# Kernel tuning notes

Hardware: AMD Instinct MI355X
Metric: run time of the kernel (lower is better)

## Reference

```python
import jax, jax.numpy as jnp
import numpy as np

N_NODES = 100000
N_EDGES = 600000
IN_FEAT = 128
OUT_FEAT = 128
NUM_RELS = 8
NUM_BASES = 4


def setup_inputs() -> dict:
    key = jax.random.key(0)
    ks = jax.random.split(key, 8)
    h = jax.random.normal(ks[0], (N_NODES, IN_FEAT), dtype=jnp.float32)
    # xavier-ish scale for params
    weight = jax.random.normal(ks[1], (NUM_BASES, IN_FEAT, OUT_FEAT), dtype=jnp.float32) * (1.0 / np.sqrt(IN_FEAT))
    w_comp = jax.random.normal(ks[2], (NUM_RELS, NUM_BASES), dtype=jnp.float32) * (1.0 / np.sqrt(NUM_BASES))
    root_weight = jax.random.normal(ks[3], (IN_FEAT, OUT_FEAT), dtype=jnp.float32) * (1.0 / np.sqrt(IN_FEAT))
    bias = jnp.zeros((OUT_FEAT,), dtype=jnp.float32)
    src = jax.random.randint(ks[4], (N_EDGES,), 0, N_NODES, dtype=jnp.int32)
    dst = jax.random.randint(ks[5], (N_EDGES,), 0, N_NODES, dtype=jnp.int32)
    rel_type = jax.random.randint(ks[6], (N_EDGES,), 0, NUM_RELS, dtype=jnp.int32)
    return {"h": h, "weight": weight, "w_comp": w_comp, "root_weight": root_weight,
            "bias": bias, "src": src, "dst": dst, "rel_type": rel_type}


def reference(h, weight, w_comp, root_weight, bias, src, dst, rel_type):
    # Basis decomposition: W[r] = sum_b w_comp[r,b] * weight[b]
    B, I, O = weight.shape
    R = w_comp.shape[0]
    W = (w_comp @ weight.reshape(B, I * O)).reshape(R, I, O)  # [R, in, out]
    # msg_e = h[src_e] @ W[rel_e]; computed as all-relation projection + gather
    # (avoids materializing [E, in, out] per-edge weights)
    proj = jnp.einsum('ni,rio->nro', h, W)          # [N, R, out]
    msg = proj[src, rel_type]                        # [E, out]
    agg = jax.ops.segment_sum(msg, dst, num_segments=h.shape[0])  # scatter-sum
    out = h @ root_weight + agg + bias
    return jax.nn.relu(out)
```

## Files before the change

### kernel.cpp

```cpp
#include <hip/hip_runtime.h>
#include <hip/hip_bf16.h>

#define N_NODES 100000
#define N_EDGES 600000
#define FEAT 128
#define NUM_RELS 8
#define NUM_BASES 4
#define NBE 2344

#define PREP_CAST 6250
#define PREP_BLDB 320
#define PREP_ZERO 392
#define PREP_GRID (PREP_CAST + PREP_BLDB + PREP_ZERO)

#define SCAN_TILES 98

typedef short bf16x8 __attribute__((ext_vector_type(8)));
typedef float f32x4  __attribute__((ext_vector_type(4)));
typedef float f32x2  __attribute__((ext_vector_type(2)));

__device__ inline short f2bf(float x) {
    __hip_bfloat16 b = __float2bfloat16(x);
    return *reinterpret_cast<short*>(&b);
}


__global__ __launch_bounds__(256) void k_prep(const float* __restrict__ h,
                                              const float* __restrict__ weight,
                                              const float* __restrict__ rw,
                                              short* __restrict__ hb,
                                              short* __restrict__ Btf,
                                              int* __restrict__ cnt,
                                              int* __restrict__ status) {
    int b = blockIdx.x;
    if (b < PREP_CAST) {
        int i = b * 256 + threadIdx.x;
        const float4* h4 = (const float4*)h;
        float4 v0 = h4[2 * i], v1 = h4[2 * i + 1];
        union { short s[8]; bf16x8 v; } u;
        u.s[0] = f2bf(v0.x); u.s[1] = f2bf(v0.y); u.s[2] = f2bf(v0.z); u.s[3] = f2bf(v0.w);
        u.s[4] = f2bf(v1.x); u.s[5] = f2bf(v1.y); u.s[6] = f2bf(v1.z); u.s[7] = f2bf(v1.w);
        ((bf16x8*)hb)[i] = u.v;
    } else if (b < PREP_CAST + PREP_BLDB) {
        int idx = (b - PREP_CAST) * 256 + threadIdx.x;
        int kc = idx >> 14;
        int e  = idx & 16383;
        int o  = e >> 7, ip = e & 127;
        float v = (kc == 0) ? rw[ip * FEAT + o]
                            : weight[(kc - 1) * FEAT * FEAT + ip * FEAT + o];
        int nt = o & 7, n16 = o >> 3;
        int ks = ip >> 5, quad = (ip >> 3) & 3, j = ip & 7;
        int lane = quad * 16 + n16;
        Btf[((kc * 4 + ks) * 8 + nt) * 512 + lane * 8 + j] = f2bf(v);
    } else {
        int i = (b - PREP_CAST - PREP_BLDB) * 256 + threadIdx.x;
        if (i < N_NODES) cnt[i] = 0;
        else if (i - N_NODES < 128) status[i - N_NODES] = 0;
    }
}

__global__ __launch_bounds__(256) void k_hist_dst(const int* __restrict__ dst,
                                                  int* __restrict__ cnt) {
    int i = blockIdx.x * 256 + threadIdx.x;
    if (i < N_EDGES) atomicAdd(&cnt[dst[i]], 1);
}

__global__ __launch_bounds__(256) void k_scan_lb(const int* __restrict__ cnt,
                                                 int* __restrict__ offs,
                                                 int* __restrict__ cursor,
                                                 int* __restrict__ status) {
    __shared__ int wsum[4];
    __shared__ int bcast;
    int bid = blockIdx.x;
    int lane = threadIdx.x & 63, wid = threadIdx.x >> 6;
    const int N4 = N_NODES / 4;
    int i4 = bid * 256 + threadIdx.x;

    const int4* cnt4 = (const int4*)cnt;
    int4 v = (i4 < N4) ? cnt4[i4] : make_int4(0, 0, 0, 0);
    int s = v.x + v.y + v.z + v.w;
    int incl = s;
#pragma unroll
    for (int d = 1; d < 64; d <<= 1) {
        int t = __shfl_up(incl, d);
        if (lane >= d) incl += t;
    }
    if (lane == 63) wsum[wid] = incl;
    __syncthreads();
    if (threadIdx.x == 0) {
        int a = 0;
#pragma unroll
        for (int w = 0; w < 4; ++w) { int x = wsum[w]; wsum[w] = a; a += x; }
        int total = a;
        __hip_atomic_store(&status[bid], (total << 2) | 1,
                           __ATOMIC_RELEASE, __HIP_MEMORY_SCOPE_AGENT);
        int excl = 0;
        for (int t = bid - 1; t >= 0; ) {
            int st = __hip_atomic_load(&status[t],
                                       __ATOMIC_ACQUIRE, __HIP_MEMORY_SCOPE_AGENT);
            if ((st & 3) == 0) { __builtin_amdgcn_s_sleep(1); continue; }
            excl += st >> 2;
            if ((st & 3) == 2) break;
            --t;
        }
        __hip_atomic_store(&status[bid], ((excl + total) << 2) | 2,
                           __ATOMIC_RELEASE, __HIP_MEMORY_SCOPE_AGENT);
        bcast = excl;
        if (bid == SCAN_TILES - 1) offs[N_NODES] = excl + total;
    }
    __syncthreads();
    int base = bcast + wsum[wid] + incl - s;
    if (i4 < N4) {
        int4 ex;
        ex.x = base;
        ex.y = base + v.x;
        ex.z = base + v.x + v.y;
        ex.w = base + v.x + v.y + v.z;
        ((int4*)offs)[i4]   = ex;
        ((int4*)cursor)[i4] = ex;
    }
}

__global__ __launch_bounds__(256) void k_scatter_sorted(const int* __restrict__ src,
                                                        const int* __restrict__ dst,
                                                        const int* __restrict__ rel,
                                                        int* __restrict__ cursor,
                                                        int* __restrict__ packed) {
    int e = blockIdx.x * 256 + threadIdx.x;
    if (e < N_EDGES) {
        int p = atomicAdd(&cursor[dst[e]], 1);
        packed[p] = (src[e] << 3) | rel[e];
    }
}

__global__ __launch_bounds__(256) void k_edge_z(const int* __restrict__ offs,
                                                const int* __restrict__ packed,
                                                const float* __restrict__ wc,
                                                const short* __restrict__ hb,
                                                unsigned int* __restrict__ z_u32) {
    int wid = threadIdx.x >> 6, lane = threadIdx.x & 63;
    int d = blockIdx.x * 4 + wid;
    if (d >= N_NODES) return;
    int s = offs[d], e = offs[d + 1];

    const float4* wc4 = (const float4*)wc;
    const unsigned int* hbu = (const unsigned int*)hb;

    f32x2 z2[4] = {(f32x2)0.f, (f32x2)0.f, (f32x2)0.f, (f32x2)0.f};

    for (int base = s; base < e; base += 64) {
        int rem = e - base;
        int m = rem < 64 ? rem : 64;
        int pk = (lane < m) ? packed[base + lane] : 0;
        int j = 0;
        for (; j + 3 < m; j += 4) {
            int p0 = __builtin_amdgcn_readlane(pk, j);
            int p1 = __builtin_amdgcn_readlane(pk, j + 1);
            int p2 = __builtin_amdgcn_readlane(pk, j + 2);
            int p3 = __builtin_amdgcn_readlane(pk, j + 3);
            unsigned int v0 = hbu[(size_t)(p0 >> 3) * 64 + lane];
            unsigned int v1 = hbu[(size_t)(p1 >> 3) * 64 + lane];
            unsigned int v2 = hbu[(size_t)(p2 >> 3) * 64 + lane];
            unsigned int v3 = hbu[(size_t)(p3 >> 3) * 64 + lane];
            float4 c0 = wc4[p0 & 7];
            float4 c1 = wc4[p1 & 7];
            float4 c2 = wc4[p2 & 7];
            float4 c3 = wc4[p3 & 7];
            f32x2 h0; h0.x = __int_as_float(v0 << 16); h0.y = __int_as_float(v0 & 0xffff0000u);
            f32x2 h1; h1.x = __int_as_float(v1 << 16); h1.y = __int_as_float(v1 & 0xffff0000u);
            f32x2 h2; h2.x = __int_as_float(v2 << 16); h2.y = __int_as_float(v2 & 0xffff0000u);
            f32x2 h3; h3.x = __int_as_float(v3 << 16); h3.y = __int_as_float(v3 & 0xffff0000u);
            f32x2 cc;
            cc = c0.x; z2[0] += cc * h0;
            cc = c0.y; z2[1] += cc * h0;
            cc = c0.z; z2[2] += cc * h0;
            cc = c0.w; z2[3] += cc * h0;
            cc = c1.x; z2[0] += cc * h1;
            cc = c1.y; z2[1] += cc * h1;
            cc = c1.z; z2[2] += cc * h1;
            cc = c1.w; z2[3] += cc * h1;
            cc = c2.x; z2[0] += cc * h2;
            cc = c2.y; z2[1] += cc * h2;
            cc = c2.z; z2[2] += cc * h2;
            cc = c2.w; z2[3] += cc * h2;
            cc = c3.x; z2[0] += cc * h3;
            cc = c3.y; z2[1] += cc * h3;
            cc = c3.z; z2[2] += cc * h3;
            cc = c3.w; z2[3] += cc * h3;
        }
        for (; j < m; ++j) {
            int p0 = __builtin_amdgcn_readlane(pk, j);
            unsigned int v0 = hbu[(size_t)(p0 >> 3) * 64 + lane];
            float4 c0 = wc4[p0 & 7];
            f32x2 h0; h0.x = __int_as_float(v0 << 16); h0.y = __int_as_float(v0 & 0xffff0000u);
            f32x2 cc;
            cc = c0.x; z2[0] += cc * h0;
            cc = c0.y; z2[1] += cc * h0;
            cc = c0.z; z2[2] += cc * h0;
            cc = c0.w; z2[3] += cc * h0;
        }
    }

    unsigned int* row = z_u32 + (size_t)d * 256;
#pragma unroll
    for (int b = 0; b < 4; ++b) {
        unsigned int lo = ((unsigned int)(unsigned short)f2bf(z2[b].x));
        unsigned int hi = ((unsigned int)(unsigned short)f2bf(z2[b].y)) << 16;
        row[b * 64 + lane] = lo | hi;
    }
}

__global__ __launch_bounds__(256) void k_gemm_fused(const short* __restrict__ hb,
                                                    const short* __restrict__ z,
                                                    const short* __restrict__ Btf,
                                                    const float* __restrict__ bias,
                                                    float* __restrict__ out) {
    __shared__ short lds[FEAT * FEAT];
    int wave = threadIdx.x >> 6, lane = threadIdx.x & 63;
    int quad = lane >> 4, n16 = lane & 15;
    int base = blockIdx.x * 64 + wave * 16;

    int rowA = base + n16;
    if (rowA >= N_NODES) rowA = N_NODES - 1;

    f32x4 acc[8];
#pragma unroll
    for (int nt = 0; nt < 8; ++nt) acc[nt] = (f32x4)0.f;

    const bf16x8* bp = (const bf16x8*)lds;
    char* lds_base = (char*)lds;

    bf16x8 a_cur[4];
    {
        const bf16x8* ap = (const bf16x8*)(hb + (size_t)rowA * FEAT);
#pragma unroll
        for (int ks = 0; ks < 4; ++ks) a_cur[ks] = ap[ks * 4 + quad];
    }

    for (int kc = 0; kc < 5; ++kc) {
        if (kc) __syncthreads();
        const char* gsrc = (const char*)Btf + kc * 32768;
#pragma unroll
        for (int t = 0; t < 8; ++t) {
            unsigned int off = wave * 8192 + t * 1024;
            __builtin_amdgcn_global_load_lds(
                (const __attribute__((address_space(1))) unsigned int*)(gsrc + off + lane * 16),
                (__attribute__((address_space(3))) unsigned int*)(lds_base + off),
                16, 0, 0);
        }
        __syncthreads();

        bf16x8 a_nxt[4];
        if (kc < 4) {
            const bf16x8* ap = (const bf16x8*)(z + (size_t)rowA * 512 + kc * FEAT);
#pragma unroll
            for (int ks = 0; ks < 4; ++ks) a_nxt[ks] = ap[ks * 4 + quad];
        }

#pragma unroll
        for (int ks = 0; ks < 4; ++ks) {
            const bf16x8* bks = bp + ks * 512 + lane;
#pragma unroll
            for (int nt = 0; nt < 8; ++nt) {
                bf16x8 b = bks[nt * 64];
                acc[nt] = __builtin_amdgcn_mfma_f32_16x16x32_bf16(a_cur[ks], b, acc[nt], 0, 0, 0);
            }
        }

        if (kc < 4) {
#pragma unroll
            for (int ks = 0; ks < 4; ++ks) a_cur[ks] = a_nxt[ks];
        }
    }

    float bv[8];
#pragma unroll
    for (int nt = 0; nt < 8; ++nt) bv[nt] = bias[n16 * 8 + nt];

#pragma unroll
    for (int reg = 0; reg < 4; ++reg) {
        int node = base + quad * 4 + reg;
        if (node < N_NODES) {
            float4 fa, fb;
            fa.x = fmaxf(acc[0][reg] + bv[0], 0.f);
            fa.y = fmaxf(acc[1][reg] + bv[1], 0.f);
            fa.z = fmaxf(acc[2][reg] + bv[2], 0.f);
            fa.w = fmaxf(acc[3][reg] + bv[3], 0.f);
            fb.x = fmaxf(acc[4][reg] + bv[4], 0.f);
            fb.y = fmaxf(acc[5][reg] + bv[5], 0.f);
            fb.z = fmaxf(acc[6][reg] + bv[6], 0.f);
            fb.w = fmaxf(acc[7][reg] + bv[7], 0.f);
            float* row = out + (size_t)node * FEAT + n16 * 8;
            *(float4*)row       = fa;
            *(float4*)(row + 4) = fb;
        }
    }
}


extern "C" void kernel_launch(void* const* d_in, const int* in_sizes, int n_in,
                              void* d_out, int out_size, void* d_ws, size_t ws_size,
                              hipStream_t stream) {
    const float* h    = (const float*)d_in[0];
    const float* wgt  = (const float*)d_in[1];
    const float* wcmp = (const float*)d_in[2];
    const float* rw   = (const float*)d_in[3];
    const float* bias = (const float*)d_in[4];
    const int*   src  = (const int*)d_in[5];
    const int*   dst  = (const int*)d_in[6];
    const int*   rel  = (const int*)d_in[7];
    float* out = (float*)d_out;

    char* ws = (char*)d_ws;
    short*        hb     = (short*)(ws + 0);
    short*        Btf    = (short*)(ws + 25600000ull);
    short*        z      = (short*)(ws + 25763840ull);
    unsigned int* z_u32  = (unsigned int*)z;
    int*          packed = (int*)(ws + 128163840ull);
    int*          cnt    = (int*)(ws + 130563840ull);
    int*          offs   = (int*)(ws + 130963840ull);
    int*          cursor = (int*)(ws + 131363968ull);
    int*          status = (int*)(ws + 131763968ull);

    hipLaunchKernelGGL(k_prep,     dim3(PREP_GRID), dim3(256), 0, stream,
                       h, wgt, rw, hb, Btf, cnt, status);
    hipLaunchKernelGGL(k_hist_dst, dim3(NBE),  dim3(256), 0, stream, dst, cnt);
    hipLaunchKernelGGL(k_scan_lb,  dim3(SCAN_TILES), dim3(256), 0, stream,
                       cnt, offs, cursor, status);
    hipLaunchKernelGGL(k_scatter_sorted, dim3(NBE), dim3(256), 0, stream,
                       src, dst, rel, cursor, packed);
    hipLaunchKernelGGL(k_edge_z,   dim3((N_NODES + 3) / 4), dim3(256), 0, stream,
                       offs, packed, wcmp, hb, z_u32);
    hipLaunchKernelGGL(k_gemm_fused, dim3((N_NODES + 63) / 64), dim3(256), 0, stream,
                       hb, z, Btf, bias, out);
}
```

Baseline: 266.6 us.

## Fuse edge aggregation into GEMM via LDS and parallelize scan lookback

The per-node basis-weighted aggregation z is now computed inside the GEMM kernel and kept in a swizzled LDS tile instead of being written to and reread from a 100000x512 bf16 global buffer. The GEMM tile shrinks to 32 rows per 512-thread block, with waves splitting the output columns. The decoupled-lookback scan now uses a full wavefront to poll 64 predecessor tiles at once instead of walking them serially with one thread. The fused kernel removes a large global write and read and a kernel launch, but it uses more LDS per block and serializes gather latency before the MFMA phase.

```diff
diff --git a/kernel.cpp b/kernel.cpp
--- a/kernel.cpp
+++ b/kernel.cpp
@@ -87,29 +87,54 @@
     }
     if (lane == 63) wsum[wid] = incl;
     __syncthreads();
-    if (threadIdx.x == 0) {
-        int a = 0;
-#pragma unroll
-        for (int w = 0; w < 4; ++w) { int x = wsum[w]; wsum[w] = a; a += x; }
-        int total = a;
-        __hip_atomic_store(&status[bid], (total << 2) | 1,
-                           __ATOMIC_RELEASE, __HIP_MEMORY_SCOPE_AGENT);
+    int total = wsum[0] + wsum[1] + wsum[2] + wsum[3];
+
+    if (threadIdx.x < 64) {
         int excl = 0;
-        for (int t = bid - 1; t >= 0; ) {
-            int st = __hip_atomic_load(&status[t],
-                                       __ATOMIC_ACQUIRE, __HIP_MEMORY_SCOPE_AGENT);
-            if ((st & 3) == 0) { __builtin_amdgcn_s_sleep(1); continue; }
-            excl += st >> 2;
-            if ((st & 3) == 2) break;
-            --t;
-        }
-        __hip_atomic_store(&status[bid], ((excl + total) << 2) | 2,
-                           __ATOMIC_RELEASE, __HIP_MEMORY_SCOPE_AGENT);
-        bcast = excl;
-        if (bid == SCAN_TILES - 1) offs[N_NODES] = excl + total;
+        if (bid > 0) {
+            if (lane == 0)
+                __hip_atomic_store(&status[bid], (total << 2) | 1,
+                                   __ATOMIC_RELEASE, __HIP_MEMORY_SCOPE_AGENT);
+            int winEnd = bid;
+            for (;;) {
+                int idx = winEnd - 64 + lane;
+                int st = 2;
+                if (idx >= 0) {
+                    st = __hip_atomic_load(&status[idx],
+                                           __ATOMIC_ACQUIRE, __HIP_MEMORY_SCOPE_AGENT);
+                    while ((st & 3) == 0) {
+                        __builtin_amdgcn_s_sleep(1);
+                        st = __hip_atomic_load(&status[idx],
+                                               __ATOMIC_ACQUIRE, __HIP_MEMORY_SCOPE_AGENT);
+                    }
+                }
+                unsigned long long done = __ballot((st & 3) == 2);
+                int contrib;
+                if (done) {
+                    int L = 63 - __builtin_clzll(done);
+                    contrib = (lane >= L) ? (st >> 2) : 0;
+                } else {
+                    contrib = st >> 2;
+                }
+#pragma unroll
+                for (int m = 1; m < 64; m <<= 1) contrib += __shfl_xor(contrib, m);
+                excl += contrib;
+                if (done) break;
+                winEnd -= 64;
+            }
+        }
+        if (lane == 0) {
+            __hip_atomic_store(&status[bid], ((excl + total) << 2) | 2,
+                               __ATOMIC_RELEASE, __HIP_MEMORY_SCOPE_AGENT);
+            bcast = excl;
+            if (bid == SCAN_TILES - 1) offs[N_NODES] = excl + total;
+        }
     }
     __syncthreads();
-    int base = bcast + wsum[wid] + incl - s;
+    int wexcl = 0;
+#pragma unroll
+    for (int w = 0; w < 4; ++w) if (w < wid) wexcl += wsum[w];
+    int base = bcast + wexcl + incl - s;
     if (i4 < N4) {
         int4 ex;
         ex.x = base;
@@ -133,102 +158,25 @@
     }
 }
 
-__global__ __launch_bounds__(256) void k_edge_z(const int* __restrict__ offs,
-                                                const int* __restrict__ packed,
-                                                const float* __restrict__ wc,
-                                                const short* __restrict__ hb,
-                                                unsigned int* __restrict__ z_u32) {
-    int wid = threadIdx.x >> 6, lane = threadIdx.x & 63;
-    int d = blockIdx.x * 4 + wid;
-    if (d >= N_NODES) return;
-    int s = offs[d], e = offs[d + 1];
-
-    const float4* wc4 = (const float4*)wc;
-    const unsigned int* hbu = (const unsigned int*)hb;
-
-    f32x2 z2[4] = {(f32x2)0.f, (f32x2)0.f, (f32x2)0.f, (f32x2)0.f};
-
-    for (int base = s; base < e; base += 64) {
-        int rem = e - base;
-        int m = rem < 64 ? rem : 64;
-        int pk = (lane < m) ? packed[base + lane] : 0;
-        int j = 0;
-        for (; j + 3 < m; j += 4) {
-            int p0 = __builtin_amdgcn_readlane(pk, j);
-            int p1 = __builtin_amdgcn_readlane(pk, j + 1);
-            int p2 = __builtin_amdgcn_readlane(pk, j + 2);
-            int p3 = __builtin_amdgcn_readlane(pk, j + 3);
-            unsigned int v0 = hbu[(size_t)(p0 >> 3) * 64 + lane];
-            unsigned int v1 = hbu[(size_t)(p1 >> 3) * 64 + lane];
-            unsigned int v2 = hbu[(size_t)(p2 >> 3) * 64 + lane];
-            unsigned int v3 = hbu[(size_t)(p3 >> 3) * 64 + lane];
-            float4 c0 = wc4[p0 & 7];
-            float4 c1 = wc4[p1 & 7];
-            float4 c2 = wc4[p2 & 7];
-            float4 c3 = wc4[p3 & 7];
-            f32x2 h0; h0.x = __int_as_float(v0 << 16); h0.y = __int_as_float(v0 & 0xffff0000u);
-            f32x2 h1; h1.x = __int_as_float(v1 << 16); h1.y = __int_as_float(v1 & 0xffff0000u);
-            f32x2 h2; h2.x = __int_as_float(v2 << 16); h2.y = __int_as_float(v2 & 0xffff0000u);
-            f32x2 h3; h3.x = __int_as_float(v3 << 16); h3.y = __int_as_float(v3 & 0xffff0000u);
-            f32x2 cc;
-            cc = c0.x; z2[0] += cc * h0;
-            cc = c0.y; z2[1] += cc * h0;
-            cc = c0.z; z2[2] += cc * h0;
-            cc = c0.w; z2[3] += cc * h0;
-            cc = c1.x; z2[0] += cc * h1;
-            cc = c1.y; z2[1] += cc * h1;
-            cc = c1.z; z2[2] += cc * h1;
-            cc = c1.w; z2[3] += cc * h1;
-            cc = c2.x; z2[0] += cc * h2;
-            cc = c2.y; z2[1] += cc * h2;
-            cc = c2.z; z2[2] += cc * h2;
-            cc = c2.w; z2[3] += cc * h2;
-            cc = c3.x; z2[0] += cc * h3;
-            cc = c3.y; z2[1] += cc * h3;
-            cc = c3.z; z2[2] += cc * h3;
-            cc = c3.w; z2[3] += cc * h3;
-        }
-        for (; j < m; ++j) {
-            int p0 = __builtin_amdgcn_readlane(pk, j);
-            unsigned int v0 = hbu[(size_t)(p0 >> 3) * 64 + lane];
-            float4 c0 = wc4[p0 & 7];
-            f32x2 h0; h0.x = __int_as_float(v0 << 16); h0.y = __int_as_float(v0 & 0xffff0000u);
-            f32x2 cc;
-            cc = c0.x; z2[0] += cc * h0;
-            cc = c0.y; z2[1] += cc * h0;
-            cc = c0.z; z2[2] += cc * h0;
-            cc = c0.w; z2[3] += cc * h0;
-        }
-    }
-
-    unsigned int* row = z_u32 + (size_t)d * 256;
-#pragma unroll
-    for (int b = 0; b < 4; ++b) {
-        unsigned int lo = ((unsigned int)(unsigned short)f2bf(z2[b].x));
-        unsigned int hi = ((unsigned int)(unsigned short)f2bf(z2[b].y)) << 16;
-        row[b * 64 + lane] = lo | hi;
-    }
-}
-
-__global__ __launch_bounds__(256) void k_gemm_fused(const short* __restrict__ hb,
-                                                    const short* __restrict__ z,
-                                                    const short* __restrict__ Btf,
-                                                    const float* __restrict__ bias,
-                                                    float* __restrict__ out) {
-    __shared__ short lds[FEAT * FEAT];
-    int wave = threadIdx.x >> 6, lane = threadIdx.x & 63;
+__global__ __launch_bounds__(512, 4) void k_edge_gemm(const int* __restrict__ offs,
+                                                      const int* __restrict__ packed,
+                                                      const float* __restrict__ wc,
+                                                      const short* __restrict__ hb,
+                                                      const short* __restrict__ Btf,
+                                                      const float* __restrict__ bias,
+                                                      float* __restrict__ out) {
+    __shared__ unsigned int zt[32 * 256];
+    __shared__ short blds[FEAT * FEAT];
+
+    int tid = threadIdx.x;
+    int wave = tid >> 6, lane = tid & 63;
     int quad = lane >> 4, n16 = lane & 15;
-    int base = blockIdx.x * 64 + wave * 16;
-
-    int rowA = base + n16;
+    int rbase = blockIdx.x * 32;
+
+    int mgrp = wave & 1, nq = wave >> 1;
+    int lrow = mgrp * 16 + n16;
+    int rowA = rbase + lrow;
     if (rowA >= N_NODES) rowA = N_NODES - 1;
-
-    f32x4 acc[8];
-#pragma unroll
-    for (int nt = 0; nt < 8; ++nt) acc[nt] = (f32x4)0.f;
-
-    const bf16x8* bp = (const bf16x8*)lds;
-    char* lds_base = (char*)lds;
 
     bf16x8 a_cur[4];
     {
@@ -237,62 +185,126 @@
         for (int ks = 0; ks < 4; ++ks) a_cur[ks] = ap[ks * 4 + quad];
     }
 
+    const float4* wc4 = (const float4*)wc;
+    const unsigned int* hbu = (const unsigned int*)hb;
+
+    for (int r4 = 0; r4 < 4; ++r4) {
+        int lr = wave * 4 + r4;
+        int d = rbase + lr;
+        if (d >= N_NODES) break;
+        int s = offs[d], e = offs[d + 1];
+
+        f32x2 z2[4] = {(f32x2)0.f, (f32x2)0.f, (f32x2)0.f, (f32x2)0.f};
+
+        for (int base = s; base < e; base += 64) {
+            int rem = e - base;
+            int m = rem < 64 ? rem : 64;
+            int pk = (lane < m) ? packed[base + lane] : 0;
+            int j = 0;
+            for (; j + 3 < m; j += 4) {
+                int p0 = __builtin_amdgcn_readlane(pk, j);
+                int p1 = __builtin_amdgcn_readlane(pk, j + 1);
+                int p2 = __builtin_amdgcn_readlane(pk, j + 2);
+                int p3 = __builtin_amdgcn_readlane(pk, j + 3);
+                unsigned int v0 = hbu[(size_t)(p0 >> 3) * 64 + lane];
+                unsigned int v1 = hbu[(size_t)(p1 >> 3) * 64 + lane];
+                unsigned int v2 = hbu[(size_t)(p2 >> 3) * 64 + lane];
+                unsigned int v3 = hbu[(size_t)(p3 >> 3) * 64 + lane];
+                float4 c0 = wc4[p0 & 7];
+                float4 c1 = wc4[p1 & 7];
+                float4 c2 = wc4[p2 & 7];
+                float4 c3 = wc4[p3 & 7];
+                f32x2 h0; h0.x = __int_as_float(v0 << 16); h0.y = __int_as_float(v0 & 0xffff0000u);
+                f32x2 h1; h1.x = __int_as_float(v1 << 16); h1.y = __int_as_float(v1 & 0xffff0000u);
+                f32x2 h2; h2.x = __int_as_float(v2 << 16); h2.y = __int_as_float(v2 & 0xffff0000u);
+                f32x2 h3; h3.x = __int_as_float(v3 << 16); h3.y = __int_as_float(v3 & 0xffff0000u);
+                f32x2 cc;
+                cc = c0.x; z2[0] += cc * h0;
+                cc = c0.y; z2[1] += cc * h0;
+                cc = c0.z; z2[2] += cc * h0;
+                cc = c0.w; z2[3] += cc * h0;
+                cc = c1.x; z2[0] += cc * h1;
+                cc = c1.y; z2[1] += cc * h1;
+                cc = c1.z; z2[2] += cc * h1;
+                cc = c1.w; z2[3] += cc * h1;
+                cc = c2.x; z2[0] += cc * h2;
+                cc = c2.y; z2[1] += cc * h2;
+                cc = c2.z; z2[2] += cc * h2;
+                cc = c2.w; z2[3] += cc * h2;
+                cc = c3.x; z2[0] += cc * h3;
+                cc = c3.y; z2[1] += cc * h3;
+                cc = c3.z; z2[2] += cc * h3;
+                cc = c3.w; z2[3] += cc * h3;
+            }
+            for (; j < m; ++j) {
+                int p0 = __builtin_amdgcn_readlane(pk, j);
+                unsigned int v0 = hbu[(size_t)(p0 >> 3) * 64 + lane];
+                float4 c0 = wc4[p0 & 7];
+                f32x2 h0; h0.x = __int_as_float(v0 << 16); h0.y = __int_as_float(v0 & 0xffff0000u);
+                f32x2 cc;
+                cc = c0.x; z2[0] += cc * h0;
+                cc = c0.y; z2[1] += cc * h0;
+                cc = c0.z; z2[2] += cc * h0;
+                cc = c0.w; z2[3] += cc * h0;
+            }
+        }
+
+        unsigned int xr = (unsigned)(lr & 7) << 2;
+#pragma unroll
+        for (int b = 0; b < 4; ++b) {
+            unsigned int lo = ((unsigned int)(unsigned short)f2bf(z2[b].x));
+            unsigned int hi = ((unsigned int)(unsigned short)f2bf(z2[b].y)) << 16;
+            zt[(lr * 256 + b * 64 + lane) ^ xr] = lo | hi;
+        }
+    }
+    __syncthreads();
+
+    f32x4 acc[2];
+    acc[0] = (f32x4)0.f; acc[1] = (f32x4)0.f;
+    const bf16x8* bp = (const bf16x8*)blds;
+    char* lds_base = (char*)blds;
+    unsigned int xrr = (unsigned)(lrow & 7) << 2;
+
     for (int kc = 0; kc < 5; ++kc) {
         if (kc) __syncthreads();
         const char* gsrc = (const char*)Btf + kc * 32768;
 #pragma unroll
-        for (int t = 0; t < 8; ++t) {
-            unsigned int off = wave * 8192 + t * 1024;
+        for (int t = 0; t < 4; ++t) {
+            unsigned int off = wave * 4096 + t * 1024;
             __builtin_amdgcn_global_load_lds(
                 (const __attribute__((address_space(1))) unsigned int*)(gsrc + off + lane * 16),
                 (__attribute__((address_space(3))) unsigned int*)(lds_base + off),
                 16, 0, 0);
         }
+        if (kc) {
+#pragma unroll
+            for (int ks = 0; ks < 4; ++ks)
+                a_cur[ks] = *(const bf16x8*)(zt +
+                    ((lrow * 256 + (kc - 1) * 64 + ks * 16 + quad * 4) ^ xrr));
+        }
         __syncthreads();
 
-        bf16x8 a_nxt[4];
-        if (kc < 4) {
-            const bf16x8* ap = (const bf16x8*)(z + (size_t)rowA * 512 + kc * FEAT);
-#pragma unroll
-            for (int ks = 0; ks < 4; ++ks) a_nxt[ks] = ap[ks * 4 + quad];
-        }
-
 #pragma unroll
         for (int ks = 0; ks < 4; ++ks) {
-            const bf16x8* bks = bp + ks * 512 + lane;
-#pragma unroll
-            for (int nt = 0; nt < 8; ++nt) {
-                bf16x8 b = bks[nt * 64];
-                acc[nt] = __builtin_amdgcn_mfma_f32_16x16x32_bf16(a_cur[ks], b, acc[nt], 0, 0, 0);
+#pragma unroll
+            for (int j = 0; j < 2; ++j) {
+                bf16x8 b = bp[(ks * 8 + nq * 2 + j) * 64 + lane];
+                acc[j] = __builtin_amdgcn_mfma_f32_16x16x32_bf16(a_cur[ks], b, acc[j], 0, 0, 0);
             }
         }
-
-        if (kc < 4) {
-#pragma unroll
-            for (int ks = 0; ks < 4; ++ks) a_cur[ks] = a_nxt[ks];
-        }
-    }
-
-    float bv[8];
-#pragma unroll
-    for (int nt = 0; nt < 8; ++nt) bv[nt] = bias[n16 * 8 + nt];
+    }
+
+    float bv0 = bias[n16 * 8 + nq * 2];
+    float bv1 = bias[n16 * 8 + nq * 2 + 1];
 
 #pragma unroll
     for (int reg = 0; reg < 4; ++reg) {
-        int node = base + quad * 4 + reg;
+        int node = rbase + mgrp * 16 + quad * 4 + reg;
         if (node < N_NODES) {
-            float4 fa, fb;
-            fa.x = fmaxf(acc[0][reg] + bv[0], 0.f);
-            fa.y = fmaxf(acc[1][reg] + bv[1], 0.f);
-            fa.z = fmaxf(acc[2][reg] + bv[2], 0.f);
-            fa.w = fmaxf(acc[3][reg] + bv[3], 0.f);
-            fb.x = fmaxf(acc[4][reg] + bv[4], 0.f);
-            fb.y = fmaxf(acc[5][reg] + bv[5], 0.f);
-            fb.z = fmaxf(acc[6][reg] + bv[6], 0.f);
-            fb.w = fmaxf(acc[7][reg] + bv[7], 0.f);
-            float* row = out + (size_t)node * FEAT + n16 * 8;
-            *(float4*)row       = fa;
-            *(float4*)(row + 4) = fb;
+            float2 f;
+            f.x = fmaxf(acc[0][reg] + bv0, 0.f);
+            f.y = fmaxf(acc[1][reg] + bv1, 0.f);
+            *(float2*)(out + (size_t)node * FEAT + n16 * 8 + nq * 2) = f;
         }
     }
 }
@@ -314,8 +326,6 @@
     char* ws = (char*)d_ws;
     short*        hb     = (short*)(ws + 0);
     short*        Btf    = (short*)(ws + 25600000ull);
-    short*        z      = (short*)(ws + 25763840ull);
-    unsigned int* z_u32  = (unsigned int*)z;
     int*          packed = (int*)(ws + 128163840ull);
     int*          cnt    = (int*)(ws + 130563840ull);
     int*          offs   = (int*)(ws + 130963840ull);
@@ -329,8 +339,6 @@
                        cnt, offs, cursor, status);
     hipLaunchKernelGGL(k_scatter_sorted, dim3(NBE), dim3(256), 0, stream,
                        src, dst, rel, cursor, packed);
-    hipLaunchKernelGGL(k_edge_z,   dim3((N_NODES + 3) / 4), dim3(256), 0, stream,
-                       offs, packed, wcmp, hb, z_u32);
-    hipLaunchKernelGGL(k_gemm_fused, dim3((N_NODES + 63) / 64), dim3(256), 0, stream,
-                       hb, z, Btf, bias, out);
-}
+    hipLaunchKernelGGL(k_edge_gemm, dim3(N_NODES / 32), dim3(512), 0, stream,
+                       offs, packed, wcmp, hb, Btf, bias, out);
+}
```

Result: slower. 272.4 us (+2.2%).

## Process two destination nodes per wave in edge gather and parallelize scan lookback

Applied to the files above, without the earlier changes.

The edge aggregation kernel now has each wave handle two destination nodes at once, interleaving their gathered h rows so twice as many independent loads are in flight per wave and the grid halves. The decoupled-lookback scan now uses a full wavefront to read 64 predecessor tile statuses in parallel and reduce them with shuffles, instead of one thread walking back serially. The two-node interleave adds more code paths and registers, which may lower occupancy. When two neighbouring nodes have very different degrees, part of the work falls back to single-stream loops.

```diff
diff --git a/kernel.cpp b/kernel.cpp
--- a/kernel.cpp
+++ b/kernel.cpp
@@ -87,29 +87,54 @@
     }
     if (lane == 63) wsum[wid] = incl;
     __syncthreads();
-    if (threadIdx.x == 0) {
-        int a = 0;
-#pragma unroll
-        for (int w = 0; w < 4; ++w) { int x = wsum[w]; wsum[w] = a; a += x; }
-        int total = a;
-        __hip_atomic_store(&status[bid], (total << 2) | 1,
-                           __ATOMIC_RELEASE, __HIP_MEMORY_SCOPE_AGENT);
+    int total = wsum[0] + wsum[1] + wsum[2] + wsum[3];
+
+    if (threadIdx.x < 64) {
         int excl = 0;
-        for (int t = bid - 1; t >= 0; ) {
-            int st = __hip_atomic_load(&status[t],
-                                       __ATOMIC_ACQUIRE, __HIP_MEMORY_SCOPE_AGENT);
-            if ((st & 3) == 0) { __builtin_amdgcn_s_sleep(1); continue; }
-            excl += st >> 2;
-            if ((st & 3) == 2) break;
-            --t;
-        }
-        __hip_atomic_store(&status[bid], ((excl + total) << 2) | 2,
-                           __ATOMIC_RELEASE, __HIP_MEMORY_SCOPE_AGENT);
-        bcast = excl;
-        if (bid == SCAN_TILES - 1) offs[N_NODES] = excl + total;
+        if (bid > 0) {
+            if (lane == 0)
+                __hip_atomic_store(&status[bid], (total << 2) | 1,
+                                   __ATOMIC_RELEASE, __HIP_MEMORY_SCOPE_AGENT);
+            int winEnd = bid;
+            for (;;) {
+                int idx = winEnd - 64 + lane;
+                int st = 2;
+                if (idx >= 0) {
+                    st = __hip_atomic_load(&status[idx],
+                                           __ATOMIC_ACQUIRE, __HIP_MEMORY_SCOPE_AGENT);
+                    while ((st & 3) == 0) {
+                        __builtin_amdgcn_s_sleep(1);
+                        st = __hip_atomic_load(&status[idx],
+                                               __ATOMIC_ACQUIRE, __HIP_MEMORY_SCOPE_AGENT);
+                    }
+                }
+                unsigned long long done = __ballot((st & 3) == 2);
+                int contrib;
+                if (done) {
+                    int L = 63 - __builtin_clzll(done);
+                    contrib = (lane >= L) ? (st >> 2) : 0;
+                } else {
+                    contrib = st >> 2;
+                }
+#pragma unroll
+                for (int m = 1; m < 64; m <<= 1) contrib += __shfl_xor(contrib, m);
+                excl += contrib;
+                if (done) break;
+                winEnd -= 64;
+            }
+        }
+        if (lane == 0) {
+            __hip_atomic_store(&status[bid], ((excl + total) << 2) | 2,
+                               __ATOMIC_RELEASE, __HIP_MEMORY_SCOPE_AGENT);
+            bcast = excl;
+            if (bid == SCAN_TILES - 1) offs[N_NODES] = excl + total;
+        }
     }
     __syncthreads();
-    int base = bcast + wsum[wid] + incl - s;
+    int wexcl = 0;
+#pragma unroll
+    for (int w = 0; w < 4; ++w) if (w < wid) wexcl += wsum[w];
+    int base = bcast + wexcl + incl - s;
     if (i4 < N4) {
         int4 ex;
         ex.x = base;
@@ -133,80 +158,116 @@
     }
 }
 
+#define RL(pk, j) __builtin_amdgcn_readlane(pk, j)
+#define EDGE_ACC(zz, c, v)                                               \
+    {   f32x2 hh; hh.x = __int_as_float((v) << 16);                      \
+        hh.y = __int_as_float((v) & 0xffff0000u);                        \
+        f32x2 cc;                                                        \
+        cc = c.x; zz[0] += cc * hh;                                      \
+        cc = c.y; zz[1] += cc * hh;                                      \
+        cc = c.z; zz[2] += cc * hh;                                      \
+        cc = c.w; zz[3] += cc * hh; }
+
 __global__ __launch_bounds__(256) void k_edge_z(const int* __restrict__ offs,
                                                 const int* __restrict__ packed,
                                                 const float* __restrict__ wc,
                                                 const short* __restrict__ hb,
                                                 unsigned int* __restrict__ z_u32) {
     int wid = threadIdx.x >> 6, lane = threadIdx.x & 63;
-    int d = blockIdx.x * 4 + wid;
-    if (d >= N_NODES) return;
-    int s = offs[d], e = offs[d + 1];
+    int d0 = blockIdx.x * 8 + wid * 2;
+    int s0 = offs[d0], sM = offs[d0 + 1], e1 = offs[d0 + 2];
 
     const float4* wc4 = (const float4*)wc;
     const unsigned int* hbu = (const unsigned int*)hb;
 
-    f32x2 z2[4] = {(f32x2)0.f, (f32x2)0.f, (f32x2)0.f, (f32x2)0.f};
-
-    for (int base = s; base < e; base += 64) {
-        int rem = e - base;
-        int m = rem < 64 ? rem : 64;
-        int pk = (lane < m) ? packed[base + lane] : 0;
-        int j = 0;
-        for (; j + 3 < m; j += 4) {
-            int p0 = __builtin_amdgcn_readlane(pk, j);
-            int p1 = __builtin_amdgcn_readlane(pk, j + 1);
-            int p2 = __builtin_amdgcn_readlane(pk, j + 2);
-            int p3 = __builtin_amdgcn_readlane(pk, j + 3);
-            unsigned int v0 = hbu[(size_t)(p0 >> 3) * 64 + lane];
-            unsigned int v1 = hbu[(size_t)(p1 >> 3) * 64 + lane];
-            unsigned int v2 = hbu[(size_t)(p2 >> 3) * 64 + lane];
-            unsigned int v3 = hbu[(size_t)(p3 >> 3) * 64 + lane];
-            float4 c0 = wc4[p0 & 7];
-            float4 c1 = wc4[p1 & 7];
-            float4 c2 = wc4[p2 & 7];
-            float4 c3 = wc4[p3 & 7];
-            f32x2 h0; h0.x = __int_as_float(v0 << 16); h0.y = __int_as_float(v0 & 0xffff0000u);
-            f32x2 h1; h1.x = __int_as_float(v1 << 16); h1.y = __int_as_float(v1 & 0xffff0000u);
-            f32x2 h2; h2.x = __int_as_float(v2 << 16); h2.y = __int_as_float(v2 & 0xffff0000u);
-            f32x2 h3; h3.x = __int_as_float(v3 << 16); h3.y = __int_as_float(v3 & 0xffff0000u);
-            f32x2 cc;
-            cc = c0.x; z2[0] += cc * h0;
-            cc = c0.y; z2[1] += cc * h0;
-            cc = c0.z; z2[2] += cc * h0;
-            cc = c0.w; z2[3] += cc * h0;
-            cc = c1.x; z2[0] += cc * h1;
-            cc = c1.y; z2[1] += cc * h1;
-            cc = c1.z; z2[2] += cc * h1;
-            cc = c1.w; z2[3] += cc * h1;
-            cc = c2.x; z2[0] += cc * h2;
-            cc = c2.y; z2[1] += cc * h2;
-            cc = c2.z; z2[2] += cc * h2;
-            cc = c2.w; z2[3] += cc * h2;
-            cc = c3.x; z2[0] += cc * h3;
-            cc = c3.y; z2[1] += cc * h3;
-            cc = c3.z; z2[2] += cc * h3;
-            cc = c3.w; z2[3] += cc * h3;
-        }
-        for (; j < m; ++j) {
-            int p0 = __builtin_amdgcn_readlane(pk, j);
-            unsigned int v0 = hbu[(size_t)(p0 >> 3) * 64 + lane];
-            float4 c0 = wc4[p0 & 7];
-            f32x2 h0; h0.x = __int_as_float(v0 << 16); h0.y = __int_as_float(v0 & 0xffff0000u);
-            f32x2 cc;
-            cc = c0.x; z2[0] += cc * h0;
-            cc = c0.y; z2[1] += cc * h0;
-            cc = c0.z; z2[2] += cc * h0;
-            cc = c0.w; z2[3] += cc * h0;
-        }
-    }
-
-    unsigned int* row = z_u32 + (size_t)d * 256;
+    f32x2 za[4] = {(f32x2)0.f, (f32x2)0.f, (f32x2)0.f, (f32x2)0.f};
+    f32x2 zb[4] = {(f32x2)0.f, (f32x2)0.f, (f32x2)0.f, (f32x2)0.f};
+
+    int baseA = s0, baseB = sM;
+    while (baseA < sM || baseB < e1) {
+        int mA = sM - baseA; mA = mA < 0 ? 0 : (mA > 64 ? 64 : mA);
+        int mB = e1 - baseB; mB = mB < 0 ? 0 : (mB > 64 ? 64 : mB);
+        int pkA = (lane < mA) ? packed[baseA + lane] : 0;
+        int pkB = (lane < mB) ? packed[baseB + lane] : 0;
+        int jA = 0, jB = 0;
+
+        while (jA + 3 < mA && jB + 3 < mB) {
+            int a0 = RL(pkA, jA), a1 = RL(pkA, jA + 1), a2 = RL(pkA, jA + 2), a3 = RL(pkA, jA + 3);
+            int b0 = RL(pkB, jB), b1 = RL(pkB, jB + 1), b2 = RL(pkB, jB + 2), b3 = RL(pkB, jB + 3);
+            unsigned int va0 = hbu[(size_t)(a0 >> 3) * 64 + lane];
+            unsigned int va1 = hbu[(size_t)(a1 >> 3) * 64 + lane];
+            unsigned int va2 = hbu[(size_t)(a2 >> 3) * 64 + lane];
+            unsigned int va3 = hbu[(size_t)(a3 >> 3) * 64 + lane];
+            unsigned int vb0 = hbu[(size_t)(b0 >> 3) * 64 + lane];
+            unsigned int vb1 = hbu[(size_t)(b1 >> 3) * 64 + lane];
+            unsigned int vb2 = hbu[(size_t)(b2 >> 3) * 64 + lane];
+            unsigned int vb3 = hbu[(size_t)(b3 >> 3) * 64 + lane];
+            float4 ca0 = wc4[a0 & 7], ca1 = wc4[a1 & 7], ca2 = wc4[a2 & 7], ca3 = wc4[a3 & 7];
+            float4 cb0 = wc4[b0 & 7], cb1 = wc4[b1 & 7], cb2 = wc4[b2 & 7], cb3 = wc4[b3 & 7];
+            EDGE_ACC(za, ca0, va0); EDGE_ACC(za, ca1, va1);
+            EDGE_ACC(za, ca2, va2); EDGE_ACC(za, ca3, va3);
+            EDGE_ACC(zb, cb0, vb0); EDGE_ACC(zb, cb1, vb1);
+            EDGE_ACC(zb, cb2, vb2); EDGE_ACC(zb, cb3, vb3);
+            jA += 4; jB += 4;
+        }
+        while (jA < mA && jB < mB) {
+            int a0 = RL(pkA, jA), b0 = RL(pkB, jB);
+            unsigned int va0 = hbu[(size_t)(a0 >> 3) * 64 + lane];
+            unsigned int vb0 = hbu[(size_t)(b0 >> 3) * 64 + lane];
+            float4 ca0 = wc4[a0 & 7], cb0 = wc4[b0 & 7];
+            EDGE_ACC(za, ca0, va0);
+            EDGE_ACC(zb, cb0, vb0);
+            ++jA; ++jB;
+        }
+        while (jA + 3 < mA) {
+            int a0 = RL(pkA, jA), a1 = RL(pkA, jA + 1), a2 = RL(pkA, jA + 2), a3 = RL(pkA, jA + 3);
+            unsigned int va0 = hbu[(size_t)(a0 >> 3) * 64 + lane];
+            unsigned int va1 = hbu[(size_t)(a1 >> 3) * 64 + lane];
+            unsigned int va2 = hbu[(size_t)(a2 >> 3) * 64 + lane];
+            unsigned int va3 = hbu[(size_t)(a3 >> 3) * 64 + lane];
+            float4 ca0 = wc4[a0 & 7], ca1 = wc4[a1 & 7], ca2 = wc4[a2 & 7], ca3 = wc4[a3 & 7];
+            EDGE_ACC(za, ca0, va0); EDGE_ACC(za, ca1, va1);
+            EDGE_ACC(za, ca2, va2); EDGE_ACC(za, ca3, va3);
+            jA += 4;
+        }
+        while (jA < mA) {
+            int a0 = RL(pkA, jA);
+            unsigned int va0 = hbu[(size_t)(a0 >> 3) * 64 + lane];
+            float4 ca0 = wc4[a0 & 7];
+            EDGE_ACC(za, ca0, va0);
+            ++jA;
+        }
+        while (jB + 3 < mB) {
+            int b0 = RL(pkB, jB), b1 = RL(pkB, jB + 1), b2 = RL(pkB, jB + 2), b3 = RL(pkB, jB + 3);
+            unsigned int vb0 = hbu[(size_t)(b0 >> 3) * 64 + lane];
+            unsigned int vb1 = hbu[(size_t)(b1 >> 3) * 64 + lane];
+            unsigned int vb2 = hbu[(size_t)(b2 >> 3) * 64 + lane];
+            unsigned int vb3 = hbu[(size_t)(b3 >> 3) * 64 + lane];
+            float4 cb0 = wc4[b0 & 7], cb1 = wc4[b1 & 7], cb2 = wc4[b2 & 7], cb3 = wc4[b3 & 7];
+            EDGE_ACC(zb, cb0, vb0); EDGE_ACC(zb, cb1, vb1);
+            EDGE_ACC(zb, cb2, vb2); EDGE_ACC(zb, cb3, vb3);
+            jB += 4;
+        }
+        while (jB < mB) {
+            int b0 = RL(pkB, jB);
+            unsigned int vb0 = hbu[(size_t)(b0 >> 3) * 64 + lane];
+            float4 cb0 = wc4[b0 & 7];
+            EDGE_ACC(zb, cb0, vb0);
+            ++jB;
+        }
+        baseA += 64; baseB += 64;
+    }
+
+    unsigned int* row0 = z_u32 + (size_t)d0 * 256;
+    unsigned int* row1 = row0 + 256;
 #pragma unroll
     for (int b = 0; b < 4; ++b) {
-        unsigned int lo = ((unsigned int)(unsigned short)f2bf(z2[b].x));
-        unsigned int hi = ((unsigned int)(unsigned short)f2bf(z2[b].y)) << 16;
-        row[b * 64 + lane] = lo | hi;
+        unsigned int lo0 = ((unsigned int)(unsigned short)f2bf(za[b].x));
+        unsigned int hi0 = ((unsigned int)(unsigned short)f2bf(za[b].y)) << 16;
+        row0[b * 64 + lane] = lo0 | hi0;
+        unsigned int lo1 = ((unsigned int)(unsigned short)f2bf(zb[b].x));
+        unsigned int hi1 = ((unsigned int)(unsigned short)f2bf(zb[b].y)) << 16;
+        row1[b * 64 + lane] = lo1 | hi1;
     }
 }
 
@@ -329,7 +390,7 @@
                        cnt, offs, cursor, status);
     hipLaunchKernelGGL(k_scatter_sorted, dim3(NBE), dim3(256), 0, stream,
                        src, dst, rel, cursor, packed);
-    hipLaunchKernelGGL(k_edge_z,   dim3((N_NODES + 3) / 4), dim3(256), 0, stream,
+    hipLaunchKernelGGL(k_edge_z,   dim3(N_NODES / 8), dim3(256), 0, stream,
                        offs, packed, wcmp, hb, z_u32);
     hipLaunchKernelGGL(k_gemm_fused, dim3((N_NODES + 63) / 64), dim3(256), 0, stream,
                        hb, z, Btf, bias, out);
```

Measured after the change: 253.6 us. 1.05x faster.
